# Kernel optimization log

Hardware: AMD Instinct MI355X
Metric: run time of the kernel (lower is better)

Reference implementation:

```python
import jax, jax.numpy as jnp
import numpy as np

NOISE_STD = 0.1
TOP_K = 2


def setup_inputs() -> dict:
    key = jax.random.key(0)
    k_x, k_n, k_w, k_keys = jax.random.split(key, 4)
    N, D_IN, D_Q, K = 16384, 2048, 256, 64
    x = jax.random.normal(k_x, (N, D_IN), dtype=jnp.float32)
    noise = jax.random.normal(k_n, (N, K), dtype=jnp.float32)
    # Linear params (kaiming-uniform-ish scale) and xavier-uniform keys
    w_q = jax.random.normal(k_w, (D_IN, D_Q), dtype=jnp.float32) * (1.0 / np.sqrt(D_IN))
    b_q = jnp.zeros((D_Q,), dtype=jnp.float32)
    lim = np.sqrt(6.0 / (K + D_Q))
    keys = jax.random.uniform(k_keys, (K, D_Q), dtype=jnp.float32, minval=-lim, maxval=lim)
    return {"x": x, "noise": noise, "w_q": w_q, "b_q": b_q, "keys": keys}


def reference(x, noise, w_q, b_q, keys):
    # query projection: [N, D_in] @ [D_in, D_q] -> [N, D_q]
    query = x @ w_q + b_q
    d_q = query.shape[-1]
    # router logits: [N, K], scaled dot product with expert keys
    logits = (query @ keys.T) * (1.0 / jnp.sqrt(jnp.asarray(d_q, query.dtype)))
    logits = logits + noise * NOISE_STD  # training-mode gating noise
    # top-k selection + softmax over selected logits only
    top_logits, top_idx = jax.lax.top_k(logits, TOP_K)       # [N, top_k]
    top_probs = jax.nn.softmax(top_logits, axis=-1)           # [N, top_k]
    # scatter selected probs into dense [N, K] gating tensor (zeros elsewhere)
    rows = jnp.arange(logits.shape[0])[:, None]               # [N, 1]
    gating_probs = jnp.zeros_like(logits).at[rows, top_idx].set(top_probs)
    return gating_probs, top_idx
```

## Files before the change

kernel.cpp:

```cpp
#include <hip/hip_runtime.h>

#define MROWS 16384
#define KD 2048
#define NQ 256
#define NE 64
#define INV_SQRT_DQ 0.0625f
#define NOISE_STD_C 0.1f

typedef _Float16 f16x8 __attribute__((ext_vector_type(8)));
typedef float f32x4 __attribute__((ext_vector_type(4)));

__device__ inline void split8v(f32x4 a, f32x4 b, f16x8* h, f16x8* l) {
    f16x8 hh, ll;
#pragma unroll
    for (int i = 0; i < 4; ++i) {
        _Float16 s = (_Float16)a[i];
        hh[i] = s; ll[i] = (_Float16)(a[i] - (float)s);
    }
#pragma unroll
    for (int i = 0; i < 4; ++i) {
        _Float16 s = (_Float16)b[i];
        hh[4 + i] = s; ll[4 + i] = (_Float16)(b[i] - (float)s);
    }
    *h = hh; *l = ll;
}

__global__ void prep_w(const float* __restrict__ w, _Float16* __restrict__ whp,
                       _Float16* __restrict__ wlp) {
    const int tid = blockIdx.x * 256 + threadIdx.x;
    const int f    = tid & 15;
    const int q    = (tid >> 4) & 3;
    const int ngrp = (tid >> 6) & 15;
    const int kcs  = tid >> 10;
    const int n = ngrp * 16 + f;
    const int k = kcs * 32 + q * 8;
    f16x8 h, l;
#pragma unroll
    for (int j = 0; j < 8; ++j) {
        float v = w[(size_t)(k + j) * NQ + n];
        _Float16 s = (_Float16)v;
        h[j] = s;
        l[j] = (_Float16)(v - (float)s);
    }
    *(f16x8*)(whp + (size_t)tid * 8) = h;
    *(f16x8*)(wlp + (size_t)tid * 8) = l;
}

__global__ __launch_bounds__(512) void gemm_fused(
    const float* __restrict__ x, const _Float16* __restrict__ whp,
    const _Float16* __restrict__ wlp, const float* __restrict__ bq,
    const float* __restrict__ keys, const float* __restrict__ noise,
    float* __restrict__ gate, float* __restrict__ idxout) {
    __shared__ __align__(16) char smem[66560];

    const int t = threadIdx.x;
    const int lane = t & 63;
    const int wv = t >> 6;
    const int m0 = blockIdx.x * 64;
    const int f = lane & 15;
    const int qq = lane >> 4;
    const int aswz = (f & 7) * 8;

    const int srow = t >> 3;
    const int sk8 = (t & 7) * 8;
    const int scol = sk8 ^ ((srow & 7) * 8);
    const f32x4* xp = (const f32x4*)(x + (size_t)(m0 + srow) * KD + sk8);

    const _Float16* bph = whp + (size_t)(2 * wv) * 512 + lane * 8;
    const _Float16* bpl = wlp + (size_t)(2 * wv) * 512 + lane * 8;

    f32x4 acc[4][2];
#pragma unroll
    for (int mt = 0; mt < 4; ++mt)
#pragma unroll
        for (int nt = 0; nt < 2; ++nt) acc[mt][nt] = {0.f, 0.f, 0.f, 0.f};

    f16x8 bhC[2][2], blC[2][2], bhN[2][2], blN[2][2];

    f32x4 xa = __builtin_nontemporal_load(xp);
    f32x4 xb = __builtin_nontemporal_load(xp + 1);
#pragma unroll
    for (int ks = 0; ks < 2; ++ks)
#pragma unroll
        for (int nt = 0; nt < 2; ++nt) {
            size_t o = (size_t)ks * 8192 + nt * 512;
            bhC[ks][nt] = *(const f16x8*)(bph + o);
            blC[ks][nt] = *(const f16x8*)(bpl + o);
        }
    {
        f16x8 h8, l8;
        split8v(xa, xb, &h8, &l8);
        *(f16x8*)((_Float16*)smem + srow * 64 + scol) = h8;
        *(f16x8*)((_Float16*)(smem + 8192) + srow * 64 + scol) = l8;
    }
    xa = __builtin_nontemporal_load(xp + 16);
    xb = __builtin_nontemporal_load(xp + 17);
    __syncthreads();

    for (int i = 0; i < 32; ++i) {
        const int cb = i & 1;
        _Float16* AhC = (_Float16*)(smem + cb * 16384);
        _Float16* AlC = AhC + 4096;
        _Float16* AhN = (_Float16*)(smem + (cb ^ 1) * 16384);
        _Float16* AlN = AhN + 4096;

        if (i + 1 < 32) {
            size_t base = (size_t)(2 * (i + 1)) * 8192;
#pragma unroll
            for (int ks = 0; ks < 2; ++ks)
#pragma unroll
                for (int nt = 0; nt < 2; ++nt) {
                    size_t o = base + (size_t)ks * 8192 + nt * 512;
                    bhN[ks][nt] = *(const f16x8*)(bph + o);
                    blN[ks][nt] = *(const f16x8*)(bpl + o);
                }
        }
        if (i + 1 < 32) {
            f16x8 h8, l8;
            split8v(xa, xb, &h8, &l8);
            *(f16x8*)(AhN + srow * 64 + scol) = h8;
            *(f16x8*)(AlN + srow * 64 + scol) = l8;
        }
        if (i + 2 < 32) {
            xa = __builtin_nontemporal_load(xp + (i + 2) * 16);
            xb = __builtin_nontemporal_load(xp + (i + 2) * 16 + 1);
        }
#pragma unroll
        for (int ks = 0; ks < 2; ++ks) {
            f16x8 ah[4], al[4];
#pragma unroll
            for (int mt = 0; mt < 4; ++mt) {
                int ab = (mt * 16 + f) * 64 + ((ks * 32 + qq * 8) ^ aswz);
                ah[mt] = *(const f16x8*)(AhC + ab);
                al[mt] = *(const f16x8*)(AlC + ab);
            }
#pragma unroll
            for (int mt = 0; mt < 4; ++mt)
#pragma unroll
                for (int nt = 0; nt < 2; ++nt) {
                    acc[mt][nt] = __builtin_amdgcn_mfma_f32_16x16x32_f16(ah[mt], bhC[ks][nt], acc[mt][nt], 0, 0, 0);
                    acc[mt][nt] = __builtin_amdgcn_mfma_f32_16x16x32_f16(ah[mt], blC[ks][nt], acc[mt][nt], 0, 0, 0);
                    acc[mt][nt] = __builtin_amdgcn_mfma_f32_16x16x32_f16(al[mt], bhC[ks][nt], acc[mt][nt], 0, 0, 0);
                }
        }
#pragma unroll
        for (int ks = 0; ks < 2; ++ks)
#pragma unroll
            for (int nt = 0; nt < 2; ++nt) {
                bhC[ks][nt] = bhN[ks][nt];
                blC[ks][nt] = blN[ks][nt];
            }
        asm volatile("" ::: "memory");
        __builtin_amdgcn_s_waitcnt(0xC07F);
        __builtin_amdgcn_s_barrier();
        asm volatile("" ::: "memory");
    }

    float* qs = (float*)smem;
#pragma unroll
    for (int nt = 0; nt < 2; ++nt) {
        int col = wv * 32 + nt * 16 + f;
        float bias = bq[col];
#pragma unroll
        for (int mt = 0; mt < 4; ++mt)
#pragma unroll
            for (int r = 0; r < 4; ++r)
                qs[(mt * 16 + qq * 4 + r) * 260 + col] = acc[mt][nt][r] + bias;
    }
    __syncthreads();

    const int e = wv * 16 + f;
    f32x4 a2[4];
#pragma unroll
    for (int mt = 0; mt < 4; ++mt) a2[mt] = {0.f, 0.f, 0.f, 0.f};
    if (wv < 4) {
        const float* kp = keys + (size_t)e * NQ + qq * 8;
        for (int kc = 0; kc < NQ; kc += 32) {
            f32x4 b0 = *(const f32x4*)(kp + kc);
            f32x4 b1 = *(const f32x4*)(kp + kc + 4);
            f16x8 bh2, bl2;
            split8v(b0, b1, &bh2, &bl2);
#pragma unroll
            for (int mt = 0; mt < 4; ++mt) {
                const float* ap = qs + (mt * 16 + f) * 260 + kc + qq * 8;
                f32x4 a0 = *(const f32x4*)ap;
                f32x4 a1 = *(const f32x4*)(ap + 4);
                f16x8 ah2, al2;
                split8v(a0, a1, &ah2, &al2);
                a2[mt] = __builtin_amdgcn_mfma_f32_16x16x32_f16(ah2, bh2, a2[mt], 0, 0, 0);
                a2[mt] = __builtin_amdgcn_mfma_f32_16x16x32_f16(ah2, bl2, a2[mt], 0, 0, 0);
                a2[mt] = __builtin_amdgcn_mfma_f32_16x16x32_f16(al2, bh2, a2[mt], 0, 0, 0);
            }
        }
    }
    __syncthreads();

    float* LG = (float*)smem;
    if (wv < 4) {
#pragma unroll
        for (int mt = 0; mt < 4; ++mt)
#pragma unroll
            for (int r = 0; r < 4; ++r) {
                int row = mt * 16 + qq * 4 + r;
                LG[row * 65 + e] = a2[mt][r] * INV_SQRT_DQ +
                                   NOISE_STD_C * noise[(size_t)(m0 + row) * NE + e];
            }
    }
    __syncthreads();

    for (int i = 0; i < 8; ++i) {
        int r = wv * 8 + i;
        float v = LG[r * 65 + lane];
        float v1 = v; int i1 = lane;
#pragma unroll
        for (int off = 32; off; off >>= 1) {
            float ov = __shfl_xor(v1, off);
            int oi = __shfl_xor(i1, off);
            if (ov > v1 || (ov == v1 && oi < i1)) { v1 = ov; i1 = oi; }
        }
        float v2 = (lane == i1) ? -1e30f : v;
        int i2 = lane;
#pragma unroll
        for (int off = 32; off; off >>= 1) {
            float ov = __shfl_xor(v2, off);
            int oi = __shfl_xor(i2, off);
            if (ov > v2 || (ov == v2 && oi < i2)) { v2 = ov; i2 = oi; }
        }
        float ex = expf(v2 - v1);
        float p1 = 1.0f / (1.0f + ex);
        float p2 = ex * p1;
        float g = (lane == i1) ? p1 : ((lane == i2) ? p2 : 0.0f);
        gate[(size_t)(m0 + r) * NE + lane] = g;
        if (lane == 0) {
            float2 ii = make_float2((float)i1, (float)i2);
            *(float2*)(idxout + (size_t)(m0 + r) * 2) = ii;
        }
    }
}

extern "C" void kernel_launch(void* const* d_in, const int* in_sizes, int n_in,
                              void* d_out, int out_size, void* d_ws, size_t ws_size,
                              hipStream_t stream) {
    const float* x     = (const float*)d_in[0];
    const float* noise = (const float*)d_in[1];
    const float* w_q   = (const float*)d_in[2];
    const float* b_q   = (const float*)d_in[3];
    const float* keys  = (const float*)d_in[4];
    float* out = (float*)d_out;

    char* ws = (char*)d_ws;
    _Float16* whp = (_Float16*)ws;
    _Float16* wlp = (_Float16*)(ws + (1u << 20));

    prep_w<<<256, 256, 0, stream>>>(w_q, whp, wlp);
    gemm_fused<<<256, 512, 0, stream>>>(x, whp, wlp, b_q, keys, noise,
                                        out, out + (size_t)MROWS * NE);
}
```

Before: 231.6 us.

## Split K across two wave groups with 32x32 MFMA tiles and reduce in LDS

```diff
diff --git a/kernel.cpp b/kernel.cpp
--- a/kernel.cpp
+++ b/kernel.cpp
@@ -9,6 +9,7 @@
 
 typedef _Float16 f16x8 __attribute__((ext_vector_type(8)));
 typedef float f32x4 __attribute__((ext_vector_type(4)));
+typedef float f32x16 __attribute__((ext_vector_type(16)));
 
 __device__ inline void split8v(f32x4 a, f32x4 b, f16x8* h, f16x8* l) {
     f16x8 hh, ll;
@@ -28,152 +29,181 @@
 __global__ void prep_w(const float* __restrict__ w, _Float16* __restrict__ whp,
                        _Float16* __restrict__ wlp) {
     const int tid = blockIdx.x * 256 + threadIdx.x;
-    const int f    = tid & 15;
-    const int q    = (tid >> 4) & 3;
-    const int ngrp = (tid >> 6) & 15;
-    const int kcs  = tid >> 10;
-    const int n = ngrp * 16 + f;
-    const int k = kcs * 32 + q * 8;
-    f16x8 h, l;
+    const int l = tid & 63;
+    const int ngrp = (tid >> 6) & 7;
+    const int K16 = tid >> 9;
+    const int n = ngrp * 32 + (l & 31);
+    const int k = K16 * 16 + (l >> 5) * 8;
+    f16x8 h, lo;
 #pragma unroll
     for (int j = 0; j < 8; ++j) {
         float v = w[(size_t)(k + j) * NQ + n];
         _Float16 s = (_Float16)v;
         h[j] = s;
-        l[j] = (_Float16)(v - (float)s);
+        lo[j] = (_Float16)(v - (float)s);
     }
     *(f16x8*)(whp + (size_t)tid * 8) = h;
-    *(f16x8*)(wlp + (size_t)tid * 8) = l;
-}
-
-__global__ __launch_bounds__(512) void gemm_fused(
+    *(f16x8*)(wlp + (size_t)tid * 8) = lo;
+}
+
+__global__ __launch_bounds__(512, 2) void gemm_fused(
     const float* __restrict__ x, const _Float16* __restrict__ whp,
     const _Float16* __restrict__ wlp, const float* __restrict__ bq,
     const float* __restrict__ keys, const float* __restrict__ noise,
     float* __restrict__ gate, float* __restrict__ idxout) {
-    __shared__ __align__(16) char smem[66560];
+    __shared__ __align__(16) char smem[83200];
 
     const int t = threadIdx.x;
     const int lane = t & 63;
     const int wv = t >> 6;
+    const int g = wv >> 2;
+    const int w = wv & 3;
     const int m0 = blockIdx.x * 64;
+
+    const int g2 = t >> 8;
+    const int tt = t & 255;
+    const int srow = tt & 63;
+    const int opair = tt >> 6;
+    const float* xs = x + (size_t)(m0 + srow) * KD + g2 * 1024 + opair * 16;
+    const int sw0 = ((opair * 2 + 0) ^ (srow & 7)) * 8;
+    const int sw1 = ((opair * 2 + 1) ^ (srow & 7)) * 8;
+    const int srowoff = srow * 64;
+    _Float16* SgBase = (_Float16*)smem + g2 * 16384;
+
+    const _Float16* bph = whp + (size_t)g * 262144 + w * 1024 + lane * 8;
+    const _Float16* bpl = wlp + (size_t)g * 262144 + w * 1024 + lane * 8;
+
+    f32x16 acc[2][2];
+#pragma unroll
+    for (int mt = 0; mt < 2; ++mt)
+#pragma unroll
+        for (int nt = 0; nt < 2; ++nt)
+#pragma unroll
+            for (int r = 0; r < 16; ++r) acc[mt][nt][r] = 0.f;
+
+    f16x8 Bh[2][2], Bl[2][2];
+
+#define BLOAD(slot, off) { \
+    Bh[slot][0] = *(const f16x8*)(bph + (off)); \
+    Bh[slot][1] = *(const f16x8*)(bph + (off) + 512); \
+    Bl[slot][0] = *(const f16x8*)(bpl + (off)); \
+    Bl[slot][1] = *(const f16x8*)(bpl + (off) + 512); }
+
+#define AREAD(T, ks, mt, ah, al) { \
+    int row_ = (mt) * 32 + (lane & 31); \
+    int so_ = ((((ks) * 2 + (lane >> 5))) ^ (row_ & 7)) * 8; \
+    ah = *(const f16x8*)((T) + row_ * 64 + so_); \
+    al = *(const f16x8*)((T) + 4096 + row_ * 64 + so_); }
+
+#define KSTEP(T, ks, slot) { \
+    f16x8 a0h, a0l, a1h, a1l; \
+    AREAD(T, ks, 0, a0h, a0l); \
+    AREAD(T, ks, 1, a1h, a1l); \
+    _Pragma("unroll") \
+    for (int nt = 0; nt < 2; ++nt) { \
+        acc[0][nt] = __builtin_amdgcn_mfma_f32_32x32x16_f16(a0h, Bh[slot][nt], acc[0][nt], 0, 0, 0); \
+        acc[0][nt] = __builtin_amdgcn_mfma_f32_32x32x16_f16(a0h, Bl[slot][nt], acc[0][nt], 0, 0, 0); \
+        acc[0][nt] = __builtin_amdgcn_mfma_f32_32x32x16_f16(a0l, Bh[slot][nt], acc[0][nt], 0, 0, 0); \
+        acc[1][nt] = __builtin_amdgcn_mfma_f32_32x32x16_f16(a1h, Bh[slot][nt], acc[1][nt], 0, 0, 0); \
+        acc[1][nt] = __builtin_amdgcn_mfma_f32_32x32x16_f16(a1h, Bl[slot][nt], acc[1][nt], 0, 0, 0); \
+        acc[1][nt] = __builtin_amdgcn_mfma_f32_32x32x16_f16(a1l, Bh[slot][nt], acc[1][nt], 0, 0, 0); \
+    } }
+
+    f32x4 x0 = __builtin_nontemporal_load((const f32x4*)xs);
+    f32x4 x1 = __builtin_nontemporal_load((const f32x4*)(xs + 4));
+    f32x4 x2 = __builtin_nontemporal_load((const f32x4*)(xs + 8));
+    f32x4 x3 = __builtin_nontemporal_load((const f32x4*)(xs + 12));
+    BLOAD(0, 0);
+    BLOAD(1, 4096);
+    {
+        f16x8 h8, l8;
+        split8v(x0, x1, &h8, &l8);
+        *(f16x8*)(SgBase + srowoff + sw0) = h8;
+        *(f16x8*)(SgBase + 4096 + srowoff + sw0) = l8;
+        split8v(x2, x3, &h8, &l8);
+        *(f16x8*)(SgBase + srowoff + sw1) = h8;
+        *(f16x8*)(SgBase + 4096 + srowoff + sw1) = l8;
+    }
+    x0 = __builtin_nontemporal_load((const f32x4*)(xs + 64));
+    x1 = __builtin_nontemporal_load((const f32x4*)(xs + 68));
+    x2 = __builtin_nontemporal_load((const f32x4*)(xs + 72));
+    x3 = __builtin_nontemporal_load((const f32x4*)(xs + 76));
+    __syncthreads();
+
+#pragma unroll 2
+    for (int i = 0; i < 16; ++i) {
+        const int cb = i & 1;
+        const _Float16* T = (const _Float16*)smem + g * 16384 + cb * 8192;
+        const size_t ib = (size_t)i * 16384;
+
+        KSTEP(T, 0, 0);
+        BLOAD(0, ib + 8192);
+        if (i < 15) {
+            f16x8 h8, l8;
+            _Float16* Sn = SgBase + (cb ^ 1) * 8192;
+            split8v(x0, x1, &h8, &l8);
+            *(f16x8*)(Sn + srowoff + sw0) = h8;
+            *(f16x8*)(Sn + 4096 + srowoff + sw0) = l8;
+            split8v(x2, x3, &h8, &l8);
+            *(f16x8*)(Sn + srowoff + sw1) = h8;
+            *(f16x8*)(Sn + 4096 + srowoff + sw1) = l8;
+        }
+        if (i < 14) {
+            x0 = __builtin_nontemporal_load((const f32x4*)(xs + (i + 2) * 64));
+            x1 = __builtin_nontemporal_load((const f32x4*)(xs + (i + 2) * 64 + 4));
+            x2 = __builtin_nontemporal_load((const f32x4*)(xs + (i + 2) * 64 + 8));
+            x3 = __builtin_nontemporal_load((const f32x4*)(xs + (i + 2) * 64 + 12));
+        }
+        KSTEP(T, 1, 1);
+        BLOAD(1, ib + 12288);
+        KSTEP(T, 2, 0);
+        if (i < 15) BLOAD(0, ib + 16384);
+        KSTEP(T, 3, 1);
+        if (i < 15) BLOAD(1, ib + 20480);
+        __builtin_amdgcn_s_waitcnt(0xC07F);
+        __builtin_amdgcn_s_barrier();
+    }
+    __syncthreads();
+
+    float* qs = (float*)smem;
+    if (g == 0) {
+#pragma unroll
+        for (int nt = 0; nt < 2; ++nt) {
+            int col = w * 64 + nt * 32 + (lane & 31);
+            float bias = bq[col];
+#pragma unroll
+            for (int mt = 0; mt < 2; ++mt)
+#pragma unroll
+                for (int r = 0; r < 16; ++r) {
+                    int row = mt * 32 + (r & 3) + 8 * (r >> 2) + 4 * (lane >> 5);
+                    qs[row * 260 + col] = acc[mt][nt][r] + bias;
+                }
+        }
+    }
+    __syncthreads();
+    if (g == 1) {
+#pragma unroll
+        for (int nt = 0; nt < 2; ++nt) {
+            int col = w * 64 + nt * 32 + (lane & 31);
+#pragma unroll
+            for (int mt = 0; mt < 2; ++mt)
+#pragma unroll
+                for (int r = 0; r < 16; ++r) {
+                    int row = mt * 32 + (r & 3) + 8 * (r >> 2) + 4 * (lane >> 5);
+                    qs[row * 260 + col] += acc[mt][nt][r];
+                }
+        }
+    }
+    __syncthreads();
+
     const int f = lane & 15;
     const int qq = lane >> 4;
-    const int aswz = (f & 7) * 8;
-
-    const int srow = t >> 3;
-    const int sk8 = (t & 7) * 8;
-    const int scol = sk8 ^ ((srow & 7) * 8);
-    const f32x4* xp = (const f32x4*)(x + (size_t)(m0 + srow) * KD + sk8);
-
-    const _Float16* bph = whp + (size_t)(2 * wv) * 512 + lane * 8;
-    const _Float16* bpl = wlp + (size_t)(2 * wv) * 512 + lane * 8;
-
-    f32x4 acc[4][2];
-#pragma unroll
-    for (int mt = 0; mt < 4; ++mt)
-#pragma unroll
-        for (int nt = 0; nt < 2; ++nt) acc[mt][nt] = {0.f, 0.f, 0.f, 0.f};
-
-    f16x8 bhC[2][2], blC[2][2], bhN[2][2], blN[2][2];
-
-    f32x4 xa = __builtin_nontemporal_load(xp);
-    f32x4 xb = __builtin_nontemporal_load(xp + 1);
-#pragma unroll
-    for (int ks = 0; ks < 2; ++ks)
-#pragma unroll
-        for (int nt = 0; nt < 2; ++nt) {
-            size_t o = (size_t)ks * 8192 + nt * 512;
-            bhC[ks][nt] = *(const f16x8*)(bph + o);
-            blC[ks][nt] = *(const f16x8*)(bpl + o);
-        }
-    {
-        f16x8 h8, l8;
-        split8v(xa, xb, &h8, &l8);
-        *(f16x8*)((_Float16*)smem + srow * 64 + scol) = h8;
-        *(f16x8*)((_Float16*)(smem + 8192) + srow * 64 + scol) = l8;
-    }
-    xa = __builtin_nontemporal_load(xp + 16);
-    xb = __builtin_nontemporal_load(xp + 17);
-    __syncthreads();
-
-    for (int i = 0; i < 32; ++i) {
-        const int cb = i & 1;
-        _Float16* AhC = (_Float16*)(smem + cb * 16384);
-        _Float16* AlC = AhC + 4096;
-        _Float16* AhN = (_Float16*)(smem + (cb ^ 1) * 16384);
-        _Float16* AlN = AhN + 4096;
-
-        if (i + 1 < 32) {
-            size_t base = (size_t)(2 * (i + 1)) * 8192;
-#pragma unroll
-            for (int ks = 0; ks < 2; ++ks)
-#pragma unroll
-                for (int nt = 0; nt < 2; ++nt) {
-                    size_t o = base + (size_t)ks * 8192 + nt * 512;
-                    bhN[ks][nt] = *(const f16x8*)(bph + o);
-                    blN[ks][nt] = *(const f16x8*)(bpl + o);
-                }
-        }
-        if (i + 1 < 32) {
-            f16x8 h8, l8;
-            split8v(xa, xb, &h8, &l8);
-            *(f16x8*)(AhN + srow * 64 + scol) = h8;
-            *(f16x8*)(AlN + srow * 64 + scol) = l8;
-        }
-        if (i + 2 < 32) {
-            xa = __builtin_nontemporal_load(xp + (i + 2) * 16);
-            xb = __builtin_nontemporal_load(xp + (i + 2) * 16 + 1);
-        }
-#pragma unroll
-        for (int ks = 0; ks < 2; ++ks) {
-            f16x8 ah[4], al[4];
-#pragma unroll
-            for (int mt = 0; mt < 4; ++mt) {
-                int ab = (mt * 16 + f) * 64 + ((ks * 32 + qq * 8) ^ aswz);
-                ah[mt] = *(const f16x8*)(AhC + ab);
-                al[mt] = *(const f16x8*)(AlC + ab);
-            }
-#pragma unroll
-            for (int mt = 0; mt < 4; ++mt)
-#pragma unroll
-                for (int nt = 0; nt < 2; ++nt) {
-                    acc[mt][nt] = __builtin_amdgcn_mfma_f32_16x16x32_f16(ah[mt], bhC[ks][nt], acc[mt][nt], 0, 0, 0);
-                    acc[mt][nt] = __builtin_amdgcn_mfma_f32_16x16x32_f16(ah[mt], blC[ks][nt], acc[mt][nt], 0, 0, 0);
-                    acc[mt][nt] = __builtin_amdgcn_mfma_f32_16x16x32_f16(al[mt], bhC[ks][nt], acc[mt][nt], 0, 0, 0);
-                }
-        }
-#pragma unroll
-        for (int ks = 0; ks < 2; ++ks)
-#pragma unroll
-            for (int nt = 0; nt < 2; ++nt) {
-                bhC[ks][nt] = bhN[ks][nt];
-                blC[ks][nt] = blN[ks][nt];
-            }
-        asm volatile("" ::: "memory");
-        __builtin_amdgcn_s_waitcnt(0xC07F);
-        __builtin_amdgcn_s_barrier();
-        asm volatile("" ::: "memory");
-    }
-
-    float* qs = (float*)smem;
-#pragma unroll
-    for (int nt = 0; nt < 2; ++nt) {
-        int col = wv * 32 + nt * 16 + f;
-        float bias = bq[col];
-#pragma unroll
-        for (int mt = 0; mt < 4; ++mt)
-#pragma unroll
-            for (int r = 0; r < 4; ++r)
-                qs[(mt * 16 + qq * 4 + r) * 260 + col] = acc[mt][nt][r] + bias;
-    }
-    __syncthreads();
-
-    const int e = wv * 16 + f;
-    f32x4 a2[4];
-#pragma unroll
-    for (int mt = 0; mt < 4; ++mt) a2[mt] = {0.f, 0.f, 0.f, 0.f};
+    const int e = (wv & 3) * 16 + f;
+    float* LG = (float*)(smem + 66560);
     if (wv < 4) {
+        f32x4 a2[4];
+#pragma unroll
+        for (int mt = 0; mt < 4; ++mt) a2[mt] = {0.f, 0.f, 0.f, 0.f};
         const float* kp = keys + (size_t)e * NQ + qq * 8;
         for (int kc = 0; kc < NQ; kc += 32) {
             f32x4 b0 = *(const f32x4*)(kp + kc);
@@ -192,11 +222,6 @@
                 a2[mt] = __builtin_amdgcn_mfma_f32_16x16x32_f16(al2, bh2, a2[mt], 0, 0, 0);
             }
         }
-    }
-    __syncthreads();
-
-    float* LG = (float*)smem;
-    if (wv < 4) {
 #pragma unroll
         for (int mt = 0; mt < 4; ++mt)
 #pragma unroll
@@ -229,8 +254,8 @@
         float ex = expf(v2 - v1);
         float p1 = 1.0f / (1.0f + ex);
         float p2 = ex * p1;
-        float g = (lane == i1) ? p1 : ((lane == i2) ? p2 : 0.0f);
-        gate[(size_t)(m0 + r) * NE + lane] = g;
+        float gpr = (lane == i1) ? p1 : ((lane == i2) ? p2 : 0.0f);
+        gate[(size_t)(m0 + r) * NE + lane] = gpr;
         if (lane == 0) {
             float2 ii = make_float2((float)i1, (float)i2);
             *(float2*)(idxout + (size_t)(m0 + r) * 2) = ii;
```

After: 277.2 us. 1.2x slower.

## Halve row tile to 32 rows per block and launch twice as many blocks

Applied to the files above, without the earlier changes.

```diff
diff --git a/kernel.cpp b/kernel.cpp
--- a/kernel.cpp
+++ b/kernel.cpp
@@ -8,6 +8,7 @@
 #define NOISE_STD_C 0.1f
 
 typedef _Float16 f16x8 __attribute__((ext_vector_type(8)));
+typedef _Float16 f16x4 __attribute__((ext_vector_type(4)));
 typedef float f32x4 __attribute__((ext_vector_type(4)));
 
 __device__ inline void split8v(f32x4 a, f32x4 b, f16x8* h, f16x8* l) {
@@ -21,6 +22,16 @@
     for (int i = 0; i < 4; ++i) {
         _Float16 s = (_Float16)b[i];
         hh[4 + i] = s; ll[4 + i] = (_Float16)(b[i] - (float)s);
+    }
+    *h = hh; *l = ll;
+}
+
+__device__ inline void split4v(f32x4 a, f16x4* h, f16x4* l) {
+    f16x4 hh, ll;
+#pragma unroll
+    for (int i = 0; i < 4; ++i) {
+        _Float16 s = (_Float16)a[i];
+        hh[i] = s; ll[i] = (_Float16)(a[i] - (float)s);
     }
     *h = hh; *l = ll;
 }
@@ -46,39 +57,72 @@
     *(f16x8*)(wlp + (size_t)tid * 8) = l;
 }
 
-__global__ __launch_bounds__(512) void gemm_fused(
+__global__ __launch_bounds__(512, 4) void gemm_fused(
     const float* __restrict__ x, const _Float16* __restrict__ whp,
     const _Float16* __restrict__ wlp, const float* __restrict__ bq,
     const float* __restrict__ keys, const float* __restrict__ noise,
     float* __restrict__ gate, float* __restrict__ idxout) {
-    __shared__ __align__(16) char smem[66560];
+    __shared__ __align__(16) char smem[41600];
 
     const int t = threadIdx.x;
     const int lane = t & 63;
     const int wv = t >> 6;
-    const int m0 = blockIdx.x * 64;
+    const int m0 = blockIdx.x * 32;
     const int f = lane & 15;
     const int qq = lane >> 4;
-    const int aswz = (f & 7) * 8;
-
-    const int srow = t >> 3;
-    const int sk8 = (t & 7) * 8;
-    const int scol = sk8 ^ ((srow & 7) * 8);
-    const f32x4* xp = (const f32x4*)(x + (size_t)(m0 + srow) * KD + sk8);
+
+    const int srow = t >> 4;
+    const int kq4 = (t & 15) * 4;
+    const float* xs = x + (size_t)(m0 + srow) * KD + kq4;
+    const int scol = (((kq4 >> 3) ^ (srow & 7)) * 8) + (kq4 & 7);
+    const int sa = srow * 64 + scol;
 
     const _Float16* bph = whp + (size_t)(2 * wv) * 512 + lane * 8;
     const _Float16* bpl = wlp + (size_t)(2 * wv) * 512 + lane * 8;
 
-    f32x4 acc[4][2];
-#pragma unroll
-    for (int mt = 0; mt < 4; ++mt)
+    f32x4 acc[2][2];
+#pragma unroll
+    for (int mt = 0; mt < 2; ++mt)
 #pragma unroll
         for (int nt = 0; nt < 2; ++nt) acc[mt][nt] = {0.f, 0.f, 0.f, 0.f};
 
     f16x8 bhC[2][2], blC[2][2], bhN[2][2], blN[2][2];
 
-    f32x4 xa = __builtin_nontemporal_load(xp);
-    f32x4 xb = __builtin_nontemporal_load(xp + 1);
+#define BLOADN(i) { \
+    size_t base_ = (size_t)(2 * (i)) * 8192; \
+    _Pragma("unroll") \
+    for (int ks = 0; ks < 2; ++ks) \
+        _Pragma("unroll") \
+        for (int nt = 0; nt < 2; ++nt) { \
+            size_t o_ = base_ + (size_t)ks * 8192 + nt * 512; \
+            bhN[ks][nt] = *(const f16x8*)(bph + o_); \
+            blN[ks][nt] = *(const f16x8*)(bpl + o_); \
+        } }
+
+#define STAGE(dstf16, xv) { \
+    f16x4 h4, l4; \
+    split4v(xv, &h4, &l4); \
+    *(f16x4*)((dstf16) + sa) = h4; \
+    *(f16x4*)((dstf16) + 2048 + sa) = l4; }
+
+#define KSTEP(T, ks) { \
+    f16x8 ah[2], al[2]; \
+    _Pragma("unroll") \
+    for (int mt = 0; mt < 2; ++mt) { \
+        int ab = (mt * 16 + f) * 64 + ((((ks) * 4 + qq) ^ (f & 7)) * 8); \
+        ah[mt] = *(const f16x8*)((T) + ab); \
+        al[mt] = *(const f16x8*)((T) + 2048 + ab); \
+    } \
+    _Pragma("unroll") \
+    for (int mt = 0; mt < 2; ++mt) \
+        _Pragma("unroll") \
+        for (int nt = 0; nt < 2; ++nt) { \
+            acc[mt][nt] = __builtin_amdgcn_mfma_f32_16x16x32_f16(ah[mt], bhC[ks][nt], acc[mt][nt], 0, 0, 0); \
+            acc[mt][nt] = __builtin_amdgcn_mfma_f32_16x16x32_f16(ah[mt], blC[ks][nt], acc[mt][nt], 0, 0, 0); \
+            acc[mt][nt] = __builtin_amdgcn_mfma_f32_16x16x32_f16(al[mt], bhC[ks][nt], acc[mt][nt], 0, 0, 0); \
+        } }
+
+    f32x4 xr = __builtin_nontemporal_load((const f32x4*)xs);
 #pragma unroll
     for (int ks = 0; ks < 2; ++ks)
 #pragma unroll
@@ -87,62 +131,21 @@
             bhC[ks][nt] = *(const f16x8*)(bph + o);
             blC[ks][nt] = *(const f16x8*)(bpl + o);
         }
-    {
-        f16x8 h8, l8;
-        split8v(xa, xb, &h8, &l8);
-        *(f16x8*)((_Float16*)smem + srow * 64 + scol) = h8;
-        *(f16x8*)((_Float16*)(smem + 8192) + srow * 64 + scol) = l8;
-    }
-    xa = __builtin_nontemporal_load(xp + 16);
-    xb = __builtin_nontemporal_load(xp + 17);
+    STAGE((_Float16*)smem, xr);
+    xr = __builtin_nontemporal_load((const f32x4*)(xs + 64));
     __syncthreads();
 
     for (int i = 0; i < 32; ++i) {
         const int cb = i & 1;
-        _Float16* AhC = (_Float16*)(smem + cb * 16384);
-        _Float16* AlC = AhC + 4096;
-        _Float16* AhN = (_Float16*)(smem + (cb ^ 1) * 16384);
-        _Float16* AlN = AhN + 4096;
-
-        if (i + 1 < 32) {
-            size_t base = (size_t)(2 * (i + 1)) * 8192;
-#pragma unroll
-            for (int ks = 0; ks < 2; ++ks)
-#pragma unroll
-                for (int nt = 0; nt < 2; ++nt) {
-                    size_t o = base + (size_t)ks * 8192 + nt * 512;
-                    bhN[ks][nt] = *(const f16x8*)(bph + o);
-                    blN[ks][nt] = *(const f16x8*)(bpl + o);
-                }
-        }
-        if (i + 1 < 32) {
-            f16x8 h8, l8;
-            split8v(xa, xb, &h8, &l8);
-            *(f16x8*)(AhN + srow * 64 + scol) = h8;
-            *(f16x8*)(AlN + srow * 64 + scol) = l8;
-        }
-        if (i + 2 < 32) {
-            xa = __builtin_nontemporal_load(xp + (i + 2) * 16);
-            xb = __builtin_nontemporal_load(xp + (i + 2) * 16 + 1);
-        }
-#pragma unroll
-        for (int ks = 0; ks < 2; ++ks) {
-            f16x8 ah[4], al[4];
-#pragma unroll
-            for (int mt = 0; mt < 4; ++mt) {
-                int ab = (mt * 16 + f) * 64 + ((ks * 32 + qq * 8) ^ aswz);
-                ah[mt] = *(const f16x8*)(AhC + ab);
-                al[mt] = *(const f16x8*)(AlC + ab);
-            }
-#pragma unroll
-            for (int mt = 0; mt < 4; ++mt)
-#pragma unroll
-                for (int nt = 0; nt < 2; ++nt) {
-                    acc[mt][nt] = __builtin_amdgcn_mfma_f32_16x16x32_f16(ah[mt], bhC[ks][nt], acc[mt][nt], 0, 0, 0);
-                    acc[mt][nt] = __builtin_amdgcn_mfma_f32_16x16x32_f16(ah[mt], blC[ks][nt], acc[mt][nt], 0, 0, 0);
-                    acc[mt][nt] = __builtin_amdgcn_mfma_f32_16x16x32_f16(al[mt], bhC[ks][nt], acc[mt][nt], 0, 0, 0);
-                }
-        }
+        const _Float16* T = (const _Float16*)smem + cb * 4096;
+        _Float16* Sn = (_Float16*)smem + (cb ^ 1) * 4096;
+
+        if (i + 1 < 32) BLOADN(i + 1);
+        if (i + 1 < 32) STAGE(Sn, xr);
+        if (i + 2 < 32)
+            xr = __builtin_nontemporal_load((const f32x4*)(xs + (i + 2) * 64));
+        KSTEP(T, 0);
+        KSTEP(T, 1);
 #pragma unroll
         for (int ks = 0; ks < 2; ++ks)
 #pragma unroll
@@ -155,6 +158,7 @@
         __builtin_amdgcn_s_barrier();
         asm volatile("" ::: "memory");
     }
+    __syncthreads();
 
     float* qs = (float*)smem;
 #pragma unroll
@@ -162,54 +166,44 @@
         int col = wv * 32 + nt * 16 + f;
         float bias = bq[col];
 #pragma unroll
-        for (int mt = 0; mt < 4; ++mt)
+        for (int mt = 0; mt < 2; ++mt)
 #pragma unroll
             for (int r = 0; r < 4; ++r)
                 qs[(mt * 16 + qq * 4 + r) * 260 + col] = acc[mt][nt][r] + bias;
     }
     __syncthreads();
 
-    const int e = wv * 16 + f;
-    f32x4 a2[4];
-#pragma unroll
-    for (int mt = 0; mt < 4; ++mt) a2[mt] = {0.f, 0.f, 0.f, 0.f};
-    if (wv < 4) {
+    const int e = (wv & 3) * 16 + f;
+    const int rh = wv >> 2;
+    float* LG = (float*)(smem + 33280);
+    {
+        f32x4 a2 = {0.f, 0.f, 0.f, 0.f};
         const float* kp = keys + (size_t)e * NQ + qq * 8;
         for (int kc = 0; kc < NQ; kc += 32) {
             f32x4 b0 = *(const f32x4*)(kp + kc);
             f32x4 b1 = *(const f32x4*)(kp + kc + 4);
             f16x8 bh2, bl2;
             split8v(b0, b1, &bh2, &bl2);
-#pragma unroll
-            for (int mt = 0; mt < 4; ++mt) {
-                const float* ap = qs + (mt * 16 + f) * 260 + kc + qq * 8;
-                f32x4 a0 = *(const f32x4*)ap;
-                f32x4 a1 = *(const f32x4*)(ap + 4);
-                f16x8 ah2, al2;
-                split8v(a0, a1, &ah2, &al2);
-                a2[mt] = __builtin_amdgcn_mfma_f32_16x16x32_f16(ah2, bh2, a2[mt], 0, 0, 0);
-                a2[mt] = __builtin_amdgcn_mfma_f32_16x16x32_f16(ah2, bl2, a2[mt], 0, 0, 0);
-                a2[mt] = __builtin_amdgcn_mfma_f32_16x16x32_f16(al2, bh2, a2[mt], 0, 0, 0);
-            }
-        }
-    }
-    __syncthreads();
-
-    float* LG = (float*)smem;
-    if (wv < 4) {
-#pragma unroll
-        for (int mt = 0; mt < 4; ++mt)
-#pragma unroll
-            for (int r = 0; r < 4; ++r) {
-                int row = mt * 16 + qq * 4 + r;
-                LG[row * 65 + e] = a2[mt][r] * INV_SQRT_DQ +
-                                   NOISE_STD_C * noise[(size_t)(m0 + row) * NE + e];
-            }
-    }
-    __syncthreads();
-
-    for (int i = 0; i < 8; ++i) {
-        int r = wv * 8 + i;
+            const float* ap = qs + (rh * 16 + f) * 260 + kc + qq * 8;
+            f32x4 a0 = *(const f32x4*)ap;
+            f32x4 a1 = *(const f32x4*)(ap + 4);
+            f16x8 ah2, al2;
+            split8v(a0, a1, &ah2, &al2);
+            a2 = __builtin_amdgcn_mfma_f32_16x16x32_f16(ah2, bh2, a2, 0, 0, 0);
+            a2 = __builtin_amdgcn_mfma_f32_16x16x32_f16(ah2, bl2, a2, 0, 0, 0);
+            a2 = __builtin_amdgcn_mfma_f32_16x16x32_f16(al2, bh2, a2, 0, 0, 0);
+        }
+#pragma unroll
+        for (int r = 0; r < 4; ++r) {
+            int row = rh * 16 + qq * 4 + r;
+            LG[row * 65 + e] = a2[r] * INV_SQRT_DQ +
+                               NOISE_STD_C * noise[(size_t)(m0 + row) * NE + e];
+        }
+    }
+    __syncthreads();
+
+    for (int i = 0; i < 4; ++i) {
+        int r = wv * 4 + i;
         float v = LG[r * 65 + lane];
         float v1 = v; int i1 = lane;
 #pragma unroll
@@ -253,6 +247,6 @@
     _Float16* wlp = (_Float16*)(ws + (1u << 20));
 
     prep_w<<<256, 256, 0, stream>>>(w_q, whp, wlp);
-    gemm_fused<<<256, 512, 0, stream>>>(x, whp, wlp, b_q, keys, noise,
+    gemm_fused<<<512, 512, 0, stream>>>(x, whp, wlp, b_q, keys, noise,
                                         out, out + (size_t)MROWS * NE);
 }
```

Result: slower. 247.3 us (+6.8%).
